# Optimization experiments

Measured on AMD Instinct MI355X. Metric: run time of the kernel, lower is better.

Reference implementation:

```python
import jax, jax.numpy as jnp
import numpy as np

N = 50000
E = 800000
D = 64


def sage_conv(x, src, dst, Wl, Wr, b, n_nodes):
    # message = x[src]; mean-aggregate by dst; then lin_l(mean) + lin_r(x) + b
    msg = x[src]                                             # [E, D] gather
    ssum = jax.ops.segment_sum(msg, dst, num_segments=n_nodes)  # [N, D]
    cnt = jax.ops.segment_sum(jnp.ones((msg.shape[0],), dtype=x.dtype), dst,
                              num_segments=n_nodes)          # [N]
    mean = ssum / jnp.maximum(cnt, 1.0)[:, None]             # scatter-mean (empty rows -> 0)
    return mean @ Wl.T + x @ Wr.T + b


def setup_inputs() -> dict:
    key = jax.random.key(0)
    ks = jax.random.split(key, 8)
    scale = 1.0 / np.sqrt(D)
    x = jax.random.normal(ks[0], (N, D), dtype=jnp.float32)
    edge_index = jax.random.randint(ks[1], (2, E), 0, N, dtype=jnp.int64)
    Wl1 = jax.random.normal(ks[2], (D, D), dtype=jnp.float32) * scale
    Wr1 = jax.random.normal(ks[3], (D, D), dtype=jnp.float32) * scale
    b1 = jnp.zeros((D,), dtype=jnp.float32)
    Wl2 = jax.random.normal(ks[4], (D, D), dtype=jnp.float32) * scale
    Wr2 = jax.random.normal(ks[5], (D, D), dtype=jnp.float32) * scale
    b2 = jnp.zeros((D,), dtype=jnp.float32)
    return {"x": x, "edge_index": edge_index, "Wl1": Wl1, "Wr1": Wr1, "b1": b1,
            "Wl2": Wl2, "Wr2": Wr2, "b2": b2}


def reference(x, edge_index, Wl1, Wr1, b1, Wl2, Wr2, b2):
    src, dst = edge_index[0], edge_index[1]
    n = x.shape[0]
    h = sage_conv(x, src, dst, Wl1, Wr1, b1, n)
    h = jax.nn.relu(h)
    out = sage_conv(h, src, dst, Wl2, Wr2, b2, n)
    return out
```

## Files before the change

kernel.cpp:

```cpp
#include <hip/hip_runtime.h>

#define D 64
#define CAP 64
#define LPAD 132
#define WPAD 136
#define NPART 8

__device__ __forceinline__ unsigned int f2bf(float f) {
    unsigned int u = __float_as_uint(f);
    return (u + 0x7fffu + ((u >> 16) & 1u)) >> 16;
}
__device__ __forceinline__ float bflo(unsigned int u) { return __uint_as_float(u << 16); }
__device__ __forceinline__ float bfhi(unsigned int u) { return __uint_as_float(u & 0xffff0000u); }

__global__ void convert_kernel(const float* __restrict__ in,
                               unsigned short* __restrict__ outh, int total4) {
    int i = blockIdx.x * blockDim.x + threadIdx.x;
    int stride = gridDim.x * blockDim.x;
    for (; i < total4; i += stride) {
        float4 v = *reinterpret_cast<const float4*>(in + (size_t)i * 4);
        uint2 p;
        p.x = f2bf(v.x) | (f2bf(v.y) << 16);
        p.y = f2bf(v.z) | (f2bf(v.w) << 16);
        *reinterpret_cast<uint2*>(outh + (size_t)i * 4) = p;
    }
}

__global__ void fill_kernel(const int* __restrict__ src, const int* __restrict__ dst,
                            int* __restrict__ cnti, int* __restrict__ eidx,
                            int E, int N) {
    int part = blockIdx.x & (NPART - 1);
    int bip  = blockIdx.x >> 3;
    int span = (N + NPART - 1) / NPART;
    int lo = part * span;
    int hi = lo + span; if (hi > N) hi = N;
    int i = bip * blockDim.x + threadIdx.x;
    int stride = (gridDim.x >> 3) * blockDim.x;
    for (; i < E; i += stride) {
        int t = dst[i];
        if (t >= lo && t < hi) {
            int pos = atomicAdd(&cnti[t], 1);
            if (pos < CAP) eidx[(size_t)t * CAP + pos] = src[i];
        }
    }
}

__device__ __forceinline__ float dot4acc(float4 a, float4 w, float c) {
    c = fmaf(a.x, w.x, c);
    c = fmaf(a.y, w.y, c);
    c = fmaf(a.z, w.z, c);
    c = fmaf(a.w, w.w, c);
    return c;
}

__global__ __launch_bounds__(256, 3) void fused_kernel(
                             const float* __restrict__ xin,
                             const unsigned short* __restrict__ gath,
                             const int* __restrict__ eidx,
                             const int* __restrict__ cnti,
                             const float* __restrict__ Wl,
                             const float* __restrict__ Wr,
                             const float* __restrict__ bias,
                             float* __restrict__ out,
                             unsigned short* __restrict__ outh,
                             int do_relu, int N) {
    __shared__ float ain[64][LPAD];
    __shared__ unsigned short wsh[64][WPAD];
    __shared__ float bsh[64];
    int tid = threadIdx.x;
    int nb = blockIdx.x * 64;

    for (int c = tid; c < 64 * 32; c += 256) {
        int d = c >> 5, kc = c & 31;
        float4 v;
        if (kc < 16) v = *reinterpret_cast<const float4*>(Wl + d * D + kc * 4);
        else         v = *reinterpret_cast<const float4*>(Wr + d * D + (kc - 16) * 4);
        uint2 p;
        p.x = f2bf(v.x) | (f2bf(v.y) << 16);
        p.y = f2bf(v.z) | (f2bf(v.w) << 16);
        *reinterpret_cast<uint2*>(&wsh[d][kc * 4]) = p;
    }
    if (tid < 64) bsh[tid] = bias[tid];

    int g = tid >> 4;
    int lane = tid & 15;
    for (int ni = 0; ni < 4; ++ni) {
        int ln = ni * 16 + g;
        int node = nb + ln; if (node >= N) node = N - 1;
        int deg = cnti[node];
        int lim = deg > CAP ? CAP : deg;
        int last = lim - 1;
        const int* ep = eidx + (size_t)node * CAP;
        float4 acc = make_float4(0.f, 0.f, 0.f, 0.f);
        for (int i = 0; i < lim; i += 8) {
            int j1 = i + 1 > last ? last : i + 1;
            int j2 = i + 2 > last ? last : i + 2;
            int j3 = i + 3 > last ? last : i + 3;
            int j4 = i + 4 > last ? last : i + 4;
            int j5 = i + 5 > last ? last : i + 5;
            int j6 = i + 6 > last ? last : i + 6;
            int j7 = i + 7 > last ? last : i + 7;
            int e0 = ep[i];  int e1 = ep[j1]; int e2 = ep[j2]; int e3 = ep[j3];
            int e4 = ep[j4]; int e5 = ep[j5]; int e6 = ep[j6]; int e7 = ep[j7];
            uint2 w0 = *reinterpret_cast<const uint2*>(gath + (size_t)e0 * D + lane * 4);
            uint2 w1 = *reinterpret_cast<const uint2*>(gath + (size_t)e1 * D + lane * 4);
            uint2 w2 = *reinterpret_cast<const uint2*>(gath + (size_t)e2 * D + lane * 4);
            uint2 w3 = *reinterpret_cast<const uint2*>(gath + (size_t)e3 * D + lane * 4);
            uint2 w4 = *reinterpret_cast<const uint2*>(gath + (size_t)e4 * D + lane * 4);
            uint2 w5 = *reinterpret_cast<const uint2*>(gath + (size_t)e5 * D + lane * 4);
            uint2 w6 = *reinterpret_cast<const uint2*>(gath + (size_t)e6 * D + lane * 4);
            uint2 w7 = *reinterpret_cast<const uint2*>(gath + (size_t)e7 * D + lane * 4);
            float m1 = (i + 1 <= last) ? 1.f : 0.f;
            float m2 = (i + 2 <= last) ? 1.f : 0.f;
            float m3 = (i + 3 <= last) ? 1.f : 0.f;
            float m4 = (i + 4 <= last) ? 1.f : 0.f;
            float m5 = (i + 5 <= last) ? 1.f : 0.f;
            float m6 = (i + 6 <= last) ? 1.f : 0.f;
            float m7 = (i + 7 <= last) ? 1.f : 0.f;
            acc.x += bflo(w0.x); acc.y += bfhi(w0.x);
            acc.z += bflo(w0.y); acc.w += bfhi(w0.y);
            acc.x = fmaf(bflo(w1.x), m1, acc.x); acc.y = fmaf(bfhi(w1.x), m1, acc.y);
            acc.z = fmaf(bflo(w1.y), m1, acc.z); acc.w = fmaf(bfhi(w1.y), m1, acc.w);
            acc.x = fmaf(bflo(w2.x), m2, acc.x); acc.y = fmaf(bfhi(w2.x), m2, acc.y);
            acc.z = fmaf(bflo(w2.y), m2, acc.z); acc.w = fmaf(bfhi(w2.y), m2, acc.w);
            acc.x = fmaf(bflo(w3.x), m3, acc.x); acc.y = fmaf(bfhi(w3.x), m3, acc.y);
            acc.z = fmaf(bflo(w3.y), m3, acc.z); acc.w = fmaf(bfhi(w3.y), m3, acc.w);
            acc.x = fmaf(bflo(w4.x), m4, acc.x); acc.y = fmaf(bfhi(w4.x), m4, acc.y);
            acc.z = fmaf(bflo(w4.y), m4, acc.z); acc.w = fmaf(bfhi(w4.y), m4, acc.w);
            acc.x = fmaf(bflo(w5.x), m5, acc.x); acc.y = fmaf(bfhi(w5.x), m5, acc.y);
            acc.z = fmaf(bflo(w5.y), m5, acc.z); acc.w = fmaf(bfhi(w5.y), m5, acc.w);
            acc.x = fmaf(bflo(w6.x), m6, acc.x); acc.y = fmaf(bfhi(w6.x), m6, acc.y);
            acc.z = fmaf(bflo(w6.y), m6, acc.z); acc.w = fmaf(bfhi(w6.y), m6, acc.w);
            acc.x = fmaf(bflo(w7.x), m7, acc.x); acc.y = fmaf(bfhi(w7.x), m7, acc.y);
            acc.z = fmaf(bflo(w7.y), m7, acc.z); acc.w = fmaf(bfhi(w7.y), m7, acc.w);
        }
        float r = 1.0f / fmaxf((float)deg, 1.0f);
        acc.x *= r; acc.y *= r; acc.z *= r; acc.w *= r;
        *reinterpret_cast<float4*>(&ain[ln][lane * 4]) = acc;
        float4 xv = *reinterpret_cast<const float4*>(xin + (size_t)node * D + lane * 4);
        *reinterpret_cast<float4*>(&ain[ln][64 + lane * 4]) = xv;
    }
    __syncthreads();

    int tx = tid & 15;
    int ty = tid >> 4;

    float4 acc0 = make_float4(0.f, 0.f, 0.f, 0.f);
    float4 acc1 = make_float4(0.f, 0.f, 0.f, 0.f);
    float4 acc2 = make_float4(0.f, 0.f, 0.f, 0.f);
    float4 acc3 = make_float4(0.f, 0.f, 0.f, 0.f);

#pragma unroll 2
    for (int kc = 0; kc < 32; ++kc) {
        float4 a0 = *reinterpret_cast<const float4*>(&ain[ty +  0][kc * 4]);
        float4 a1 = *reinterpret_cast<const float4*>(&ain[ty + 16][kc * 4]);
        float4 a2 = *reinterpret_cast<const float4*>(&ain[ty + 32][kc * 4]);
        float4 a3 = *reinterpret_cast<const float4*>(&ain[ty + 48][kc * 4]);
        uint2 q0 = *reinterpret_cast<const uint2*>(&wsh[tx +  0][kc * 4]);
        uint2 q1 = *reinterpret_cast<const uint2*>(&wsh[tx + 16][kc * 4]);
        uint2 q2 = *reinterpret_cast<const uint2*>(&wsh[tx + 32][kc * 4]);
        uint2 q3 = *reinterpret_cast<const uint2*>(&wsh[tx + 48][kc * 4]);
        float4 w0 = make_float4(bflo(q0.x), bfhi(q0.x), bflo(q0.y), bfhi(q0.y));
        float4 w1 = make_float4(bflo(q1.x), bfhi(q1.x), bflo(q1.y), bfhi(q1.y));
        float4 w2 = make_float4(bflo(q2.x), bfhi(q2.x), bflo(q2.y), bfhi(q2.y));
        float4 w3 = make_float4(bflo(q3.x), bfhi(q3.x), bflo(q3.y), bfhi(q3.y));
        acc0.x = dot4acc(a0, w0, acc0.x); acc0.y = dot4acc(a0, w1, acc0.y);
        acc0.z = dot4acc(a0, w2, acc0.z); acc0.w = dot4acc(a0, w3, acc0.w);
        acc1.x = dot4acc(a1, w0, acc1.x); acc1.y = dot4acc(a1, w1, acc1.y);
        acc1.z = dot4acc(a1, w2, acc1.z); acc1.w = dot4acc(a1, w3, acc1.w);
        acc2.x = dot4acc(a2, w0, acc2.x); acc2.y = dot4acc(a2, w1, acc2.y);
        acc2.z = dot4acc(a2, w2, acc2.z); acc2.w = dot4acc(a2, w3, acc2.w);
        acc3.x = dot4acc(a3, w0, acc3.x); acc3.y = dot4acc(a3, w1, acc3.y);
        acc3.z = dot4acc(a3, w2, acc3.z); acc3.w = dot4acc(a3, w3, acc3.w);
    }

    float b0 = bsh[tx], b1 = bsh[tx + 16], b2 = bsh[tx + 32], b3 = bsh[tx + 48];
#define STORE_ROW(ACCV, I)                                                    \
    {                                                                         \
        int node = nb + ty + 16 * (I);                                        \
        if (node < N) {                                                       \
            float v0 = ACCV.x + b0, v1 = ACCV.y + b1,                         \
                  v2 = ACCV.z + b2, v3 = ACCV.w + b3;                         \
            if (do_relu) {                                                    \
                v0 = fmaxf(v0, 0.f); v1 = fmaxf(v1, 0.f);                     \
                v2 = fmaxf(v2, 0.f); v3 = fmaxf(v3, 0.f);                     \
            }                                                                 \
            float* op = out + (size_t)node * D;                               \
            op[tx] = v0; op[tx + 16] = v1; op[tx + 32] = v2; op[tx + 48] = v3;\
            if (outh) {                                                       \
                unsigned short* oh = outh + (size_t)node * D;                 \
                oh[tx]      = (unsigned short)f2bf(v0);                       \
                oh[tx + 16] = (unsigned short)f2bf(v1);                       \
                oh[tx + 32] = (unsigned short)f2bf(v2);                       \
                oh[tx + 48] = (unsigned short)f2bf(v3);                       \
            }                                                                 \
        }                                                                     \
    }
    STORE_ROW(acc0, 0)
    STORE_ROW(acc1, 1)
    STORE_ROW(acc2, 2)
    STORE_ROW(acc3, 3)
#undef STORE_ROW
}

extern "C" void kernel_launch(void* const* d_in, const int* in_sizes, int n_in,
                              void* d_out, int out_size, void* d_ws, size_t ws_size,
                              hipStream_t stream) {
    const float* x   = (const float*)d_in[0];
    const int*   ei  = (const int*)d_in[1];
    const float* Wl1 = (const float*)d_in[2];
    const float* Wr1 = (const float*)d_in[3];
    const float* b1  = (const float*)d_in[4];
    const float* Wl2 = (const float*)d_in[5];
    const float* Wr2 = (const float*)d_in[6];
    const float* b2  = (const float*)d_in[7];

    int N_ = in_sizes[0] / D;
    int E_ = in_sizes[1] / 2;
    const int* src = ei;
    const int* dst = ei + E_;

    int*            cnti = (int*)d_ws;
    int*            eidx = cnti + N_;
    float*          h    = (float*)(eidx + (size_t)N_ * CAP);
    unsigned short* xh   = (unsigned short*)(h + (size_t)N_ * D);
    unsigned short* hh   = xh + (size_t)N_ * D;
    float* outp = (float*)d_out;

    hipMemsetAsync(cnti, 0, (size_t)N_ * sizeof(int), stream);
    convert_kernel<<<2048, 256, 0, stream>>>(x, xh, N_ * D / 4);
    fill_kernel<<<2048, 256, 0, stream>>>(src, dst, cnti, eidx, E_, N_);

    int blocks = (N_ + 63) / 64;
    fused_kernel<<<blocks, 256, 0, stream>>>(x, xh, eidx, cnti, Wl1, Wr1, b1, h, hh, 1, N_);
    fused_kernel<<<blocks, 256, 0, stream>>>(h, hh, eidx, cnti, Wl2, Wr2, b2, outp,
                                             (unsigned short*)nullptr, 0, N_);
}
```

Baseline: 221.6 us.

## Use bf16 for self features and LDS operand tile, drop fp32 hidden buffer

Result: faster. 212.1 us (-4.3%).

```diff
diff --git a/kernel.cpp b/kernel.cpp
--- a/kernel.cpp
+++ b/kernel.cpp
@@ -2,7 +2,6 @@
 
 #define D 64
 #define CAP 64
-#define LPAD 132
 #define WPAD 136
 #define NPART 8
 
@@ -53,18 +52,17 @@
     return c;
 }
 
-__global__ __launch_bounds__(256, 3) void fused_kernel(
-                             const float* __restrict__ xin,
+__global__ __launch_bounds__(256, 4) void fused_kernel(
                              const unsigned short* __restrict__ gath,
                              const int* __restrict__ eidx,
                              const int* __restrict__ cnti,
                              const float* __restrict__ Wl,
                              const float* __restrict__ Wr,
                              const float* __restrict__ bias,
-                             float* __restrict__ out,
+                             float* __restrict__ outf,
                              unsigned short* __restrict__ outh,
                              int do_relu, int N) {
-    __shared__ float ain[64][LPAD];
+    __shared__ unsigned short ain[64][WPAD];
     __shared__ unsigned short wsh[64][WPAD];
     __shared__ float bsh[64];
     int tid = threadIdx.x;
@@ -92,53 +90,32 @@
         int last = lim - 1;
         const int* ep = eidx + (size_t)node * CAP;
         float4 acc = make_float4(0.f, 0.f, 0.f, 0.f);
-        for (int i = 0; i < lim; i += 8) {
-            int j1 = i + 1 > last ? last : i + 1;
-            int j2 = i + 2 > last ? last : i + 2;
-            int j3 = i + 3 > last ? last : i + 3;
-            int j4 = i + 4 > last ? last : i + 4;
-            int j5 = i + 5 > last ? last : i + 5;
-            int j6 = i + 6 > last ? last : i + 6;
-            int j7 = i + 7 > last ? last : i + 7;
-            int e0 = ep[i];  int e1 = ep[j1]; int e2 = ep[j2]; int e3 = ep[j3];
-            int e4 = ep[j4]; int e5 = ep[j5]; int e6 = ep[j6]; int e7 = ep[j7];
-            uint2 w0 = *reinterpret_cast<const uint2*>(gath + (size_t)e0 * D + lane * 4);
-            uint2 w1 = *reinterpret_cast<const uint2*>(gath + (size_t)e1 * D + lane * 4);
-            uint2 w2 = *reinterpret_cast<const uint2*>(gath + (size_t)e2 * D + lane * 4);
-            uint2 w3 = *reinterpret_cast<const uint2*>(gath + (size_t)e3 * D + lane * 4);
-            uint2 w4 = *reinterpret_cast<const uint2*>(gath + (size_t)e4 * D + lane * 4);
-            uint2 w5 = *reinterpret_cast<const uint2*>(gath + (size_t)e5 * D + lane * 4);
-            uint2 w6 = *reinterpret_cast<const uint2*>(gath + (size_t)e6 * D + lane * 4);
-            uint2 w7 = *reinterpret_cast<const uint2*>(gath + (size_t)e7 * D + lane * 4);
-            float m1 = (i + 1 <= last) ? 1.f : 0.f;
-            float m2 = (i + 2 <= last) ? 1.f : 0.f;
-            float m3 = (i + 3 <= last) ? 1.f : 0.f;
-            float m4 = (i + 4 <= last) ? 1.f : 0.f;
-            float m5 = (i + 5 <= last) ? 1.f : 0.f;
-            float m6 = (i + 6 <= last) ? 1.f : 0.f;
-            float m7 = (i + 7 <= last) ? 1.f : 0.f;
-            acc.x += bflo(w0.x); acc.y += bfhi(w0.x);
-            acc.z += bflo(w0.y); acc.w += bfhi(w0.y);
-            acc.x = fmaf(bflo(w1.x), m1, acc.x); acc.y = fmaf(bfhi(w1.x), m1, acc.y);
-            acc.z = fmaf(bflo(w1.y), m1, acc.z); acc.w = fmaf(bfhi(w1.y), m1, acc.w);
-            acc.x = fmaf(bflo(w2.x), m2, acc.x); acc.y = fmaf(bfhi(w2.x), m2, acc.y);
-            acc.z = fmaf(bflo(w2.y), m2, acc.z); acc.w = fmaf(bfhi(w2.y), m2, acc.w);
-            acc.x = fmaf(bflo(w3.x), m3, acc.x); acc.y = fmaf(bfhi(w3.x), m3, acc.y);
-            acc.z = fmaf(bflo(w3.y), m3, acc.z); acc.w = fmaf(bfhi(w3.y), m3, acc.w);
-            acc.x = fmaf(bflo(w4.x), m4, acc.x); acc.y = fmaf(bfhi(w4.x), m4, acc.y);
-            acc.z = fmaf(bflo(w4.y), m4, acc.z); acc.w = fmaf(bfhi(w4.y), m4, acc.w);
-            acc.x = fmaf(bflo(w5.x), m5, acc.x); acc.y = fmaf(bfhi(w5.x), m5, acc.y);
-            acc.z = fmaf(bflo(w5.y), m5, acc.z); acc.w = fmaf(bfhi(w5.y), m5, acc.w);
-            acc.x = fmaf(bflo(w6.x), m6, acc.x); acc.y = fmaf(bfhi(w6.x), m6, acc.y);
-            acc.z = fmaf(bflo(w6.y), m6, acc.z); acc.w = fmaf(bfhi(w6.y), m6, acc.w);
-            acc.x = fmaf(bflo(w7.x), m7, acc.x); acc.y = fmaf(bfhi(w7.x), m7, acc.y);
-            acc.z = fmaf(bflo(w7.y), m7, acc.z); acc.w = fmaf(bfhi(w7.y), m7, acc.w);
+        for (int i = 0; i < lim; i += 16) {
+#define IDX(J) int e##J = ep[(i + J > last) ? last : (i + J)];
+            IDX(0)  IDX(1)  IDX(2)  IDX(3)  IDX(4)  IDX(5)  IDX(6)  IDX(7)
+            IDX(8)  IDX(9)  IDX(10) IDX(11) IDX(12) IDX(13) IDX(14) IDX(15)
+#undef IDX
+#define LD(J) uint2 w##J = *reinterpret_cast<const uint2*>(gath + (size_t)e##J * D + lane * 4);
+            LD(0)  LD(1)  LD(2)  LD(3)  LD(4)  LD(5)  LD(6)  LD(7)
+            LD(8)  LD(9)  LD(10) LD(11) LD(12) LD(13) LD(14) LD(15)
+#undef LD
+#define ACC(J) { float m = (i + J <= last) ? 1.f : 0.f;                         \
+                 acc.x = fmaf(bflo(w##J.x), m, acc.x);                          \
+                 acc.y = fmaf(bfhi(w##J.x), m, acc.y);                          \
+                 acc.z = fmaf(bflo(w##J.y), m, acc.z);                          \
+                 acc.w = fmaf(bfhi(w##J.y), m, acc.w); }
+            ACC(0)  ACC(1)  ACC(2)  ACC(3)  ACC(4)  ACC(5)  ACC(6)  ACC(7)
+            ACC(8)  ACC(9)  ACC(10) ACC(11) ACC(12) ACC(13) ACC(14) ACC(15)
+#undef ACC
         }
         float r = 1.0f / fmaxf((float)deg, 1.0f);
         acc.x *= r; acc.y *= r; acc.z *= r; acc.w *= r;
-        *reinterpret_cast<float4*>(&ain[ln][lane * 4]) = acc;
-        float4 xv = *reinterpret_cast<const float4*>(xin + (size_t)node * D + lane * 4);
-        *reinterpret_cast<float4*>(&ain[ln][64 + lane * 4]) = xv;
+        uint2 mp;
+        mp.x = f2bf(acc.x) | (f2bf(acc.y) << 16);
+        mp.y = f2bf(acc.z) | (f2bf(acc.w) << 16);
+        *reinterpret_cast<uint2*>(&ain[ln][lane * 4]) = mp;
+        uint2 sv = *reinterpret_cast<const uint2*>(gath + (size_t)node * D + lane * 4);
+        *reinterpret_cast<uint2*>(&ain[ln][64 + lane * 4]) = sv;
     }
     __syncthreads();
 
@@ -152,18 +129,22 @@
 
 #pragma unroll 2
     for (int kc = 0; kc < 32; ++kc) {
-        float4 a0 = *reinterpret_cast<const float4*>(&ain[ty +  0][kc * 4]);
-        float4 a1 = *reinterpret_cast<const float4*>(&ain[ty + 16][kc * 4]);
-        float4 a2 = *reinterpret_cast<const float4*>(&ain[ty + 32][kc * 4]);
-        float4 a3 = *reinterpret_cast<const float4*>(&ain[ty + 48][kc * 4]);
-        uint2 q0 = *reinterpret_cast<const uint2*>(&wsh[tx +  0][kc * 4]);
-        uint2 q1 = *reinterpret_cast<const uint2*>(&wsh[tx + 16][kc * 4]);
-        uint2 q2 = *reinterpret_cast<const uint2*>(&wsh[tx + 32][kc * 4]);
-        uint2 q3 = *reinterpret_cast<const uint2*>(&wsh[tx + 48][kc * 4]);
-        float4 w0 = make_float4(bflo(q0.x), bfhi(q0.x), bflo(q0.y), bfhi(q0.y));
-        float4 w1 = make_float4(bflo(q1.x), bfhi(q1.x), bflo(q1.y), bfhi(q1.y));
-        float4 w2 = make_float4(bflo(q2.x), bfhi(q2.x), bflo(q2.y), bfhi(q2.y));
-        float4 w3 = make_float4(bflo(q3.x), bfhi(q3.x), bflo(q3.y), bfhi(q3.y));
+        uint2 qa0 = *reinterpret_cast<const uint2*>(&ain[ty +  0][kc * 4]);
+        uint2 qa1 = *reinterpret_cast<const uint2*>(&ain[ty + 16][kc * 4]);
+        uint2 qa2 = *reinterpret_cast<const uint2*>(&ain[ty + 32][kc * 4]);
+        uint2 qa3 = *reinterpret_cast<const uint2*>(&ain[ty + 48][kc * 4]);
+        uint2 qw0 = *reinterpret_cast<const uint2*>(&wsh[tx +  0][kc * 4]);
+        uint2 qw1 = *reinterpret_cast<const uint2*>(&wsh[tx + 16][kc * 4]);
+        uint2 qw2 = *reinterpret_cast<const uint2*>(&wsh[tx + 32][kc * 4]);
+        uint2 qw3 = *reinterpret_cast<const uint2*>(&wsh[tx + 48][kc * 4]);
+        float4 a0 = make_float4(bflo(qa0.x), bfhi(qa0.x), bflo(qa0.y), bfhi(qa0.y));
+        float4 a1 = make_float4(bflo(qa1.x), bfhi(qa1.x), bflo(qa1.y), bfhi(qa1.y));
+        float4 a2 = make_float4(bflo(qa2.x), bfhi(qa2.x), bflo(qa2.y), bfhi(qa2.y));
+        float4 a3 = make_float4(bflo(qa3.x), bfhi(qa3.x), bflo(qa3.y), bfhi(qa3.y));
+        float4 w0 = make_float4(bflo(qw0.x), bfhi(qw0.x), bflo(qw0.y), bfhi(qw0.y));
+        float4 w1 = make_float4(bflo(qw1.x), bfhi(qw1.x), bflo(qw1.y), bfhi(qw1.y));
+        float4 w2 = make_float4(bflo(qw2.x), bfhi(qw2.x), bflo(qw2.y), bfhi(qw2.y));
+        float4 w3 = make_float4(bflo(qw3.x), bfhi(qw3.x), bflo(qw3.y), bfhi(qw3.y));
         acc0.x = dot4acc(a0, w0, acc0.x); acc0.y = dot4acc(a0, w1, acc0.y);
         acc0.z = dot4acc(a0, w2, acc0.z); acc0.w = dot4acc(a0, w3, acc0.w);
         acc1.x = dot4acc(a1, w0, acc1.x); acc1.y = dot4acc(a1, w1, acc1.y);
@@ -185,8 +166,11 @@
                 v0 = fmaxf(v0, 0.f); v1 = fmaxf(v1, 0.f);                     \
                 v2 = fmaxf(v2, 0.f); v3 = fmaxf(v3, 0.f);                     \
             }                                                                 \
-            float* op = out + (size_t)node * D;                               \
-            op[tx] = v0; op[tx + 16] = v1; op[tx + 32] = v2; op[tx + 48] = v3;\
+            if (outf) {                                                       \
+                float* op = outf + (size_t)node * D;                          \
+                op[tx] = v0; op[tx + 16] = v1;                                \
+                op[tx + 32] = v2; op[tx + 48] = v3;                           \
+            }                                                                 \
             if (outh) {                                                       \
                 unsigned short* oh = outh + (size_t)node * D;                 \
                 oh[tx]      = (unsigned short)f2bf(v0);                       \
@@ -222,8 +206,7 @@
 
     int*            cnti = (int*)d_ws;
     int*            eidx = cnti + N_;
-    float*          h    = (float*)(eidx + (size_t)N_ * CAP);
-    unsigned short* xh   = (unsigned short*)(h + (size_t)N_ * D);
+    unsigned short* xh   = (unsigned short*)(eidx + (size_t)N_ * CAP);
     unsigned short* hh   = xh + (size_t)N_ * D;
     float* outp = (float*)d_out;
 
@@ -232,7 +215,8 @@
     fill_kernel<<<2048, 256, 0, stream>>>(src, dst, cnti, eidx, E_, N_);
 
     int blocks = (N_ + 63) / 64;
-    fused_kernel<<<blocks, 256, 0, stream>>>(x, xh, eidx, cnti, Wl1, Wr1, b1, h, hh, 1, N_);
-    fused_kernel<<<blocks, 256, 0, stream>>>(h, hh, eidx, cnti, Wl2, Wr2, b2, outp,
-                                             (unsigned short*)nullptr, 0, N_);
-}
+    fused_kernel<<<blocks, 256, 0, stream>>>(xh, eidx, cnti, Wl1, Wr1, b1,
+                                             (float*)nullptr, hh, 1, N_);
+    fused_kernel<<<blocks, 256, 0, stream>>>(hh, eidx, cnti, Wl2, Wr2, b2,
+                                             outp, (unsigned short*)nullptr, 0, N_);
+}
```
